# Performance work log

Measured on AMD Instinct MI355X. Metric: run time of the kernel, lower is better.

Reference implementation:

```python
import jax, jax.numpy as jnp
import numpy as np

N_NODES = 2048
N_EDGES = 32768
DIM = 256
HEADS = 4

PARAM_SHAPES = {
    'Wq': (DIM, DIM), 'bq': (DIM,), 'Wk': (DIM, DIM), 'bk': (DIM,),
    'Wv': (DIM, DIM), 'bv': (DIM,), 'Wo': (DIM, DIM), 'bo': (DIM,),
    'gd_W1': (4, 3), 'gd_b1': (3,), 'gd_W2': (3, HEADS), 'gd_b2': (HEADS,),
    'tw_W1': (2 * DIM, DIM), 'tw_b1': (DIM,), 'tw_W2': (DIM, DIM), 'tw_b2': (DIM,),
    'ne_W1': (4 * DIM, 2 * DIM), 'ne_b1': (2 * DIM,), 'ne_W2': (2 * DIM, DIM), 'ne_b2': (DIM,),
    'att_W1': (2 * DIM // HEADS, 2 * DIM // HEADS), 'att_b1': (2 * DIM // HEADS,),
    'att_W2': (DIM // HEADS, 2 * DIM // HEADS), 'att_b2': (DIM // HEADS,),
    'pe_W': (DIM, DIM), 'pe_b': (DIM,), 'pq_W': (DIM, DIM), 'pq_b': (DIM,),
    'pv_W': (DIM, DIM), 'pv_b': (DIM,),
    'pr_W1': (2 * DIM, 2 * DIM), 'pr_b1': (2 * DIM,), 'pr_W2': (2 * DIM, DIM), 'pr_b2': (DIM,),
}


def _lin(x, W, b):
    return x @ W + b


def _mlp2(x, W1, b1, W2, b2):  # Linear-ReLU-Linear (build_mlp, on_last=False)
    return _lin(jnp.maximum(_lin(x, W1, b1), 0.0), W2, b2)


def setup_inputs() -> dict:
    key = jax.random.key(0)
    ks = iter(jax.random.split(key, 64))
    rng = np.random.default_rng(0)
    half = N_EDGES // 2
    s = rng.integers(0, N_NODES, half)
    d = rng.integers(0, N_NODES, half)
    # reciprocal edge pairs so the reverse-edge lookup path is exercised
    edge_index = jnp.asarray(np.stack([np.concatenate([s, d]), np.concatenate([d, s])]), dtype=jnp.int32)
    inp = {
        'node_f': jax.random.normal(next(ks), (N_NODES, DIM), jnp.float32),
        'edge_f': jax.random.normal(next(ks), (N_EDGES, DIM), jnp.float32),
        'coords': jax.random.normal(next(ks), (N_NODES, 3), jnp.float32),
        'edge_index': edge_index,
        'num_heads': HEADS,
    }
    for name, shp in PARAM_SHAPES.items():
        inp[name] = jax.random.normal(next(ks), shp, jnp.float32) * 0.02
    return inp


def _forward(node_f, edge_f, coords, edge_index, num_heads,
             Wq, bq, Wk, bk, Wv, bv, Wo, bo,
             gd_W1, gd_b1, gd_W2, gd_b2,
             tw_W1, tw_b1, tw_W2, tw_b2,
             ne_W1, ne_b1, ne_W2, ne_b2,
             att_W1, att_b1, att_W2, att_b2,
             pe_W, pe_b, pq_W, pq_b, pv_W, pv_b,
             pr_W1, pr_b1, pr_W2, pr_b2):
    N, Dn = node_f.shape
    E, De = edge_f.shape
    H = num_heads
    dh = Wq.shape[1] // H
    src, dst = edge_index[0], edge_index[1]

    # --- NodeUpdate: distance-aware MHSA over all node pairs (batch=1) ---
    q = _lin(node_f, Wq, bq).reshape(N, H, dh)
    k = _lin(node_f, Wk, bk).reshape(N, H, dh)
    v = _lin(node_f, Wv, bv).reshape(N, H, dh)
    diff = coords[:, None, :] - coords[None, :, :]  # [N,N,3]
    sq = jnp.sum(diff * diff, axis=-1, keepdims=True)
    dist = jnp.where(sq > 0, jnp.sqrt(jnp.where(sq > 0, sq, 1.0)), 0.0)
    dmask = _mlp2(jnp.concatenate([diff, dist], -1), gd_W1, gd_b1, gd_W2, gd_b2)  # [N,N,H]
    scores = jnp.einsum('nhd,mhd->hnm', q, k) / float(dh) ** 0.5 + dmask.transpose(2, 0, 1)
    attn = jax.nn.softmax(scores, axis=-1)
    mhsa = _lin(jnp.einsum('hnm,mhd->nhd', attn, v).reshape(N, H * dh), Wo, bo)

    # --- TwinningEdgeAttention: per-node mean of outgoing / incoming edge feats ---
    ones = jnp.ones((E,), edge_f.dtype)
    cnt_s = jnp.maximum(jax.ops.segment_sum(ones, src, num_segments=N), 1.0)
    cnt_d = jnp.maximum(jax.ops.segment_sum(ones, dst, num_segments=N), 1.0)
    sub_mean = jax.ops.segment_sum(edge_f, src, num_segments=N) / cnt_s[:, None]
    obj_mean = jax.ops.segment_sum(edge_f, dst, num_segments=N) / cnt_d[:, None]
    edge_att = jax.nn.sigmoid(_mlp2(jnp.concatenate([sub_mean, obj_mean], -1), tw_W1, tw_b1, tw_W2, tw_b2))
    node_out = jnp.maximum(mhsa, 0.0) * edge_att  # [N, Dn]

    # --- GraphEdgeAttenNetwork ---
    x_i = node_f[src]
    x_j = node_f[dst]
    # reverse-edge matching (vectorized replacement of the python double loop)
    table = jnp.zeros((N * N,), jnp.int32).at[src * N + dst].set(jnp.arange(E, dtype=jnp.int32) + 1)
    rev = table[dst * N + src]
    rev_feat = jnp.where((rev > 0)[:, None], edge_f[jnp.maximum(rev - 1, 0)], 0.0)
    edge_out = _mlp2(jnp.concatenate([x_i, edge_f, rev_feat, x_j], -1), ne_W1, ne_b1, ne_W2, ne_b2)

    value = _lin(x_j, pv_W, pv_b)  # [E, Da]
    query = _lin(x_i, pq_W, pq_b).reshape(E, Dn // H, H)
    edgep = _lin(edge_f, pe_W, pe_b).reshape(E, De // H, H)
    qe = jnp.concatenate([query, edgep], axis=1)  # [E, d_n+d_e, H]
    # conv1d(kernel=1) MLP over channel axis, ReLU between layers
    h = jnp.maximum(jnp.einsum('ech,oc->eoh', qe, att_W1) + att_b1[None, :, None], 0.0)
    prob = jax.nn.softmax(jnp.einsum('ech,oc->eoh', h, att_W2) + att_b2[None, :, None], axis=1)  # [E, d_o, H]
    msg = prob.reshape(E, -1) * value
    agg = jax.ops.segment_max(msg, src, num_segments=N)
    agg = jnp.where(jnp.isfinite(agg), agg, 0.0)  # empty segments -> 0 (torch scatter_max fill)
    xx = _mlp2(jnp.concatenate([node_f, agg], -1), pr_W1, pr_b1, pr_W2, pr_b2)
    return node_out, edge_out, xx


def reference(node_f, edge_f, coords, edge_index, num_heads,
              Wq, bq, Wk, bk, Wv, bv, Wo, bo,
              gd_W1, gd_b1, gd_W2, gd_b2,
              tw_W1, tw_b1, tw_W2, tw_b2,
              ne_W1, ne_b1, ne_W2, ne_b2,
              att_W1, att_b1, att_W2, att_b2,
              pe_W, pe_b, pq_W, pq_b, pv_W, pv_b,
              pr_W1, pr_b1, pr_W2, pr_b2):
    return _forward(node_f, edge_f, coords, edge_index, num_heads,
                    Wq, bq, Wk, bk, Wv, bv, Wo, bo,
                    gd_W1, gd_b1, gd_W2, gd_b2,
                    tw_W1, tw_b1, tw_W2, tw_b2,
                    ne_W1, ne_b1, ne_W2, ne_b2,
                    att_W1, att_b1, att_W2, att_b2,
                    pe_W, pe_b, pq_W, pq_b, pv_W, pv_b,
                    pr_W1, pr_b1, pr_W2, pr_b2)
```

## Files before the change

kernel.cpp:

```cpp
#include <hip/hip_runtime.h>

#define NN 2048
#define NE 32768
#define DIM 256
#define NH 4

typedef unsigned short u16;
typedef __attribute__((ext_vector_type(4))) unsigned short u16x4;
typedef __attribute__((ext_vector_type(8))) short bf16x8;
typedef __attribute__((ext_vector_type(4))) float f32x4;

typedef __attribute__((address_space(1))) const unsigned int g_as1;
typedef __attribute__((address_space(3))) unsigned int l_as3;

__device__ __forceinline__ void gload16(const u16* g, u16* l) {
  __builtin_amdgcn_global_load_lds((g_as1*)g, (l_as3*)l, 16, 0, 0);
}

__device__ __forceinline__ u16 f2bf(float f) {
  unsigned u = __float_as_uint(f);
  unsigned r = u + 0x7FFFu + ((u >> 16) & 1u);
  return (u16)(r >> 16);
}
__device__ __forceinline__ float bf2f(u16 b) {
  return __uint_as_float(((unsigned)b) << 16);
}

struct GB { const u16* A; const int* idx; long ld; long aoffz; };

template<int BNF, int EPI>
__global__ __launch_bounds__(256) void gemm_bf(
    GB ga, const u16* __restrict__ Bt, long bld, long boffz,
    const float* __restrict__ bias, void* __restrict__ Cp, long ldc, long coffz,
    int K, float scale)
{
  __shared__ u16 As[128 * 64];
  __shared__ u16 Bs[32 * BNF * 64];

  const int tid = threadIdx.x;
  const int wid = tid >> 6, lane = tid & 63;
  const int bz = blockIdx.z;
  const int m0 = blockIdx.y * 128;
  const int n0 = blockIdx.x * (32 * BNF);
  const int wr = wid >> 1, wc = wid & 1;
  const int l15 = lane & 15, l4 = lane >> 4;

  const u16* asrc[4];
  #pragma unroll
  for (int c = 0; c < 4; ++c) {
    int rl = c*32 + wid*8 + (lane >> 3);
    int row = ga.idx ? ga.idx[m0 + rl] : (m0 + rl);
    int c16s = (lane & 7) ^ (rl & 7);
    asrc[c] = ga.A + ga.aoffz * bz + (long)row * ga.ld + c16s * 8;
  }
  const u16* bsrc[BNF];
  #pragma unroll
  for (int c = 0; c < BNF; ++c) {
    int rl = c*32 + wid*8 + (lane >> 3);
    int c16s = (lane & 7) ^ (rl & 7);
    bsrc[c] = Bt + boffz * bz + (long)(n0 + rl) * bld + c16s * 8;
  }

  f32x4 acc[4][BNF] = {};

  for (int k0 = 0; k0 < K; k0 += 64) {
    #pragma unroll
    for (int c = 0; c < 4; ++c)
      gload16(asrc[c] + k0, &As[(c*32 + wid*8) * 64]);
    #pragma unroll
    for (int c = 0; c < BNF; ++c)
      gload16(bsrc[c] + k0, &Bs[(c*32 + wid*8) * 64]);
    __syncthreads();

    #pragma unroll
    for (int kk = 0; kk < 2; ++kk) {
      bf16x8 af[4], bfr[BNF];
      #pragma unroll
      for (int i = 0; i < 4; ++i) {
        int r = wr*64 + i*16 + l15;
        af[i] = *(const bf16x8*)&As[r*64 + (((kk*4 + l4) ^ (r & 7)) * 8)];
      }
      #pragma unroll
      for (int j = 0; j < BNF; ++j) {
        int r = wc*(16*BNF) + j*16 + l15;
        bfr[j] = *(const bf16x8*)&Bs[r*64 + (((kk*4 + l4) ^ (r & 7)) * 8)];
      }
      #pragma unroll
      for (int i = 0; i < 4; ++i)
        #pragma unroll
        for (int j = 0; j < BNF; ++j)
          acc[i][j] = __builtin_amdgcn_mfma_f32_16x16x32_bf16(af[i], bfr[j], acc[i][j], 0, 0, 0);
    }
    __syncthreads();
  }

  #pragma unroll
  for (int j = 0; j < BNF; ++j) {
    const int col = n0 + wc*(16*BNF) + j*16 + l15;
    const float bb = bias ? bias[col] : 0.f;
    #pragma unroll
    for (int i = 0; i < 4; ++i) {
      #pragma unroll
      for (int r = 0; r < 4; ++r) {
        const int m = m0 + wr*64 + i*16 + l4*4 + r;
        float v = acc[i][j][r] * scale + bb;
        if constexpr (EPI == 1) v = fmaxf(v, 0.f);
        if constexpr (EPI == 2) v = 1.f / (1.f + expf(-v));
        if constexpr (EPI == 0 || EPI == 2)
          ((float*)Cp)[coffz*bz + (long)m*ldc + col] = v;
        else if constexpr (EPI == 4)
          ((u16*)Cp)[((long)(col & 3) * NE + m) * ldc + (col >> 2) + coffz] = f2bf(v);
        else if constexpr (EPI == 8) {
          if (col < 256)
            ((float*)Cp)[(long)m*256 + (col & 3)*64 + (col >> 2)] = v;
          else {
            u16* qb = (u16*)((float*)Cp + (long)NN*256);
            int c2 = col - 256;
            qb[((long)(c2 & 3)*NN + m)*64 + (c2 >> 2)] = f2bf(v);
          }
        }
        else
          ((u16*)Cp)[coffz*bz + (long)m*ldc + col] = f2bf(v);
      }
    }
  }
}

__global__ __launch_bounds__(256) void flash_k(
    const u16* __restrict__ qkv,
    const u16* __restrict__ vT,
    const float4* __restrict__ pk,
    const float* __restrict__ gW1, const float* __restrict__ gb1,
    const float* __restrict__ gW2, const float* __restrict__ gb2,
    u16* __restrict__ Op,
    float2* __restrict__ ml)
{
  __shared__ u16 Kls[128*64];
  __shared__ u16 Vls[2][64*64];
  __shared__ u16 Pls[4][16*128];

  const int tid = threadIdx.x, wid = tid >> 6, lane = tid & 63;
  const int h  = blockIdx.x & 3;
  const int m0 = (blockIdx.x >> 2) * 64;
  const int part = blockIdx.y;
  const int l15 = lane & 15, l4 = lane >> 4;
  const int rl8 = wid*8 + (lane >> 3);
  const int c8  = lane & 7;

  bf16x8 qf[2];
  {
    const u16* qp = qkv + (long)(m0 + wid*16 + l15)*768 + h*64 + l4*8;
    qf[0] = *(const bf16x8*)(qp);
    qf[1] = *(const bf16x8*)(qp + 32);
  }

  const float b10 = gb1[0], b11 = gb1[1], b12 = gb1[2];
  const float w30 = gW1[9], w31 = gW1[10], w32 = gW1[11];
  const float w20 = gW2[0*4+h], w21 = gW2[1*4+h], w22 = gW2[2*4+h];
  const float b2h = gb2[h];
  float4 rp0[4], rp1[4];
  #pragma unroll
  for (int r = 0; r < 4; ++r) {
    int qrow = m0 + wid*16 + l4*4 + r;
    rp0[r] = pk[qrow*2]; rp1[r] = pk[qrow*2 + 1];
  }

  float mrun[4] = {-1e30f, -1e30f, -1e30f, -1e30f};
  float lrun[4] = {};
  f32x4 pa[4] = {};

  for (int t = 0; t < 2; ++t) {
    const int n0 = part*256 + t*128;
    #pragma unroll
    for (int c = 0; c < 4; ++c) {
      int r = c*32 + rl8;
      gload16(qkv + (long)(n0 + r)*768 + 256 + h*64 + ((c8 ^ (r & 7))*8),
              &Kls[(c*32 + wid*8)*64]);
    }
    #pragma unroll
    for (int hh = 0; hh < 2; ++hh)
      #pragma unroll
      for (int c = 0; c < 2; ++c) {
        int r = c*32 + rl8;
        gload16(vT + (long)(h*64 + r)*NN + n0 + hh*64 + ((c8 ^ (r & 7))*8),
                &Vls[hh][(c*32 + wid*8)*64]);
      }
    __syncthreads();

    f32x4 sa[8] = {};
    #pragma unroll
    for (int kk = 0; kk < 2; ++kk) {
      #pragma unroll
      for (int j = 0; j < 8; ++j) {
        int r = j*16 + l15;
        bf16x8 bf = *(const bf16x8*)&Kls[r*64 + (((kk*4 + l4) ^ (r & 7))*8)];
        sa[j] = __builtin_amdgcn_mfma_f32_16x16x32_bf16(qf[kk], bf, sa[j], 0, 0, 0);
      }
    }

    float rowmx[4] = {-1e30f, -1e30f, -1e30f, -1e30f};
    #pragma unroll
    for (int j = 0; j < 8; ++j) {
      int n = n0 + j*16 + l15;
      float4 cp0 = pk[n*2], cp1 = pk[n*2 + 1];
      #pragma unroll
      for (int r = 0; r < 4; ++r) {
        float dot = rp0[r].x*cp0.x + rp0[r].y*cp0.y + rp0[r].z*cp0.z;
        float sq = rp0[r].w + cp0.w - 2.f*dot;
        float dist = sq > 0.f ? sq * __frsqrt_rn(sq) : 0.f;
        float h0 = fmaxf(b10 + rp1[r].x - cp1.x + dist*w30, 0.f);
        float h1 = fmaxf(b11 + rp1[r].y - cp1.y + dist*w31, 0.f);
        float h2 = fmaxf(b12 + rp1[r].z - cp1.z + dist*w32, 0.f);
        float s = sa[j][r]*0.125f + b2h + h0*w20 + h1*w21 + h2*w22;
        sa[j][r] = s;
        rowmx[r] = fmaxf(rowmx[r], s);
      }
    }
    #pragma unroll
    for (int w = 1; w < 16; w <<= 1)
      #pragma unroll
      for (int r = 0; r < 4; ++r)
        rowmx[r] = fmaxf(rowmx[r], __shfl_xor(rowmx[r], w));

    float fac[4], rs[4] = {};
    #pragma unroll
    for (int r = 0; r < 4; ++r) {
      float mnew = fmaxf(mrun[r], rowmx[r]);
      fac[r] = __expf(mrun[r] - mnew);
      mrun[r] = mnew;
    }
    #pragma unroll
    for (int j = 0; j < 8; ++j)
      #pragma unroll
      for (int r = 0; r < 4; ++r) {
        float p = __expf(sa[j][r] - mrun[r]);
        sa[j][r] = p;
        rs[r] += p;
      }
    #pragma unroll
    for (int w = 1; w < 16; w <<= 1)
      #pragma unroll
      for (int r = 0; r < 4; ++r)
        rs[r] += __shfl_xor(rs[r], w);
    #pragma unroll
    for (int r = 0; r < 4; ++r) lrun[r] = lrun[r]*fac[r] + rs[r];
    #pragma unroll
    for (int j2 = 0; j2 < 4; ++j2)
      #pragma unroll
      for (int r = 0; r < 4; ++r)
        pa[j2][r] *= fac[r];

    #pragma unroll
    for (int j = 0; j < 8; ++j)
      #pragma unroll
      for (int r = 0; r < 4; ++r) {
        int qr = l4*4 + r, n = j*16 + l15;
        Pls[wid][qr*128 + (((n >> 3) ^ (qr & 7))*8) + (n & 7)] = f2bf(sa[j][r]);
      }
    #pragma unroll
    for (int ks = 0; ks < 4; ++ks) {
      bf16x8 paf = *(const bf16x8*)&Pls[wid][l15*128 + (((ks*4 + l4) ^ (l15 & 7))*8)];
      #pragma unroll
      for (int j2 = 0; j2 < 4; ++j2) {
        int r = j2*16 + l15;
        bf16x8 vf = *(const bf16x8*)&Vls[ks >> 1][r*64 + ((((ks & 1)*4 + l4) ^ (r & 7))*8)];
        pa[j2] = __builtin_amdgcn_mfma_f32_16x16x32_bf16(paf, vf, pa[j2], 0, 0, 0);
      }
    }
    __syncthreads();
  }

  #pragma unroll
  for (int j2 = 0; j2 < 4; ++j2)
    #pragma unroll
    for (int r = 0; r < 4; ++r) {
      int m = m0 + wid*16 + l4*4 + r;
      Op[((long)part*NN + m)*256 + h*64 + j2*16 + l15] = f2bf(pa[j2][r]);
    }
  if (l15 == 0) {
    #pragma unroll
    for (int r = 0; r < 4; ++r) {
      int m = m0 + wid*16 + l4*4 + r;
      ml[((long)part*NN + m)*4 + h] = make_float2(mrun[r], lrun[r]);
    }
  }
}

__global__ __launch_bounds__(256) void comb_k(const u16* __restrict__ Op,
    const float2* __restrict__ ml, u16* __restrict__ attn) {
  int n = blockIdx.x, t = threadIdx.x, h = t >> 6;
  float m[8], l[8];
  #pragma unroll
  for (int p = 0; p < 8; ++p) { float2 v = ml[((long)p*NN + n)*4 + h]; m[p] = v.x; l[p] = v.y; }
  float M = m[0];
  #pragma unroll
  for (int p = 1; p < 8; ++p) M = fmaxf(M, m[p]);
  float L = 0.f, o = 0.f;
  #pragma unroll
  for (int p = 0; p < 8; ++p) {
    float w = __expf(m[p] - M);
    L += w * l[p];
    o += w * bf2f(Op[((long)p*NN + n)*256 + t]);
  }
  attn[(long)n*256 + t] = f2bf(o / L);
}

__global__ __launch_bounds__(64) void attedge_k(
    const u16* __restrict__ qN, const u16* __restrict__ ep,
    const float* __restrict__ valNp, const int* __restrict__ ei,
    const u16* __restrict__ W1, const float* __restrict__ b1,
    const u16* __restrict__ W2, const float* __restrict__ b2,
    u16* __restrict__ msgP)
{
  __shared__ u16 As[32*128];
  const int lane = threadIdx.x;
  const int h = blockIdx.y;
  const int e0 = blockIdx.x * 32;
  const int l15 = lane & 15, l4 = lane >> 4;

  #pragma unroll
  for (int p = 0; p < 8; ++p) {
    int R0 = p*4;
    int r  = R0 + (lane >> 4);
    int cd = lane & 15;
    int cs = ((cd & 7) ^ (r & 7)) | (cd & 8);
    const u16* src = (cs < 8)
        ? qN + ((long)h*NN + ei[e0 + r])*64 + cs*8
        : ep + ((long)h*NE + e0 + r)*64 + (cs & 7)*8;
    gload16(src, &As[R0*128]);
  }
  __syncthreads();

  f32x4 acc1[2][8] = {};
  #pragma unroll
  for (int kk = 0; kk < 4; ++kk) {
    bf16x8 af[2], bfr[8];
    #pragma unroll
    for (int i = 0; i < 2; ++i) {
      int rA = i*16 + l15;
      int cg = kk*4 + l4;
      int cd = ((cg & 7) ^ (rA & 7)) | (cg & 8);
      af[i] = *(const bf16x8*)&As[rA*128 + cd*8];
    }
    #pragma unroll
    for (int j = 0; j < 8; ++j)
      bfr[j] = *(const bf16x8*)&W1[(long)(j*16 + l15)*128 + kk*32 + l4*8];
    #pragma unroll
    for (int i = 0; i < 2; ++i)
      #pragma unroll
      for (int j = 0; j < 8; ++j)
        acc1[i][j] = __builtin_amdgcn_mfma_f32_16x16x32_bf16(af[i], bfr[j], acc1[i][j], 0, 0, 0);
  }
  __syncthreads();
  #pragma unroll
  for (int i = 0; i < 2; ++i)
    #pragma unroll
    for (int j = 0; j < 8; ++j) {
      int n = j*16 + l15;
      float bb = b1[n];
      #pragma unroll
      for (int r = 0; r < 4; ++r) {
        int m = i*16 + l4*4 + r;
        int cg = n >> 3;
        int cd = ((cg & 7) ^ (m & 7)) | (cg & 8);
        As[m*128 + cd*8 + (n & 7)] = f2bf(fmaxf(acc1[i][j][r] + bb, 0.f));
      }
    }
  __syncthreads();

  f32x4 acc2[2][4] = {};
  #pragma unroll
  for (int kk = 0; kk < 4; ++kk) {
    bf16x8 af[2], bfr[4];
    #pragma unroll
    for (int i = 0; i < 2; ++i) {
      int rA = i*16 + l15;
      int cg = kk*4 + l4;
      int cd = ((cg & 7) ^ (rA & 7)) | (cg & 8);
      af[i] = *(const bf16x8*)&As[rA*128 + cd*8];
    }
    #pragma unroll
    for (int j = 0; j < 4; ++j)
      bfr[j] = *(const bf16x8*)&W2[(long)(j*16 + l15)*128 + kk*32 + l4*8];
    #pragma unroll
    for (int i = 0; i < 2; ++i)
      #pragma unroll
      for (int j = 0; j < 4; ++j)
        acc2[i][j] = __builtin_amdgcn_mfma_f32_16x16x32_bf16(af[i], bfr[j], acc2[i][j], 0, 0, 0);
  }

  #pragma unroll
  for (int i = 0; i < 2; ++i) {
    float mx[4] = {-1e30f,-1e30f,-1e30f,-1e30f};
    #pragma unroll
    for (int j = 0; j < 4; ++j) {
      float bb = b2[j*16 + l15];
      #pragma unroll
      for (int r = 0; r < 4; ++r) {
        acc2[i][j][r] += bb;
        mx[r] = fmaxf(mx[r], acc2[i][j][r]);
      }
    }
    #pragma unroll
    for (int w = 1; w < 16; w <<= 1)
      #pragma unroll
      for (int r = 0; r < 4; ++r) mx[r] = fmaxf(mx[r], __shfl_xor(mx[r], w));
    float sum[4] = {};
    #pragma unroll
    for (int j = 0; j < 4; ++j)
      #pragma unroll
      for (int r = 0; r < 4; ++r) {
        float p = __expf(acc2[i][j][r] - mx[r]);
        acc2[i][j][r] = p; sum[r] += p;
      }
    #pragma unroll
    for (int w = 1; w < 16; w <<= 1)
      #pragma unroll
      for (int r = 0; r < 4; ++r) sum[r] += __shfl_xor(sum[r], w);
    #pragma unroll
    for (int r = 0; r < 4; ++r) {
      int m = i*16 + l4*4 + r;
      int e = e0 + m;
      int dst = ei[NE + e];
      float inv = 1.f / sum[r];
      #pragma unroll
      for (int j = 0; j < 4; ++j) {
        int o = j*16 + l15;
        float v = valNp[(long)dst*256 + h*64 + o];
        msgP[(long)e*256 + h*64 + o] = f2bf(acc2[i][j][r] * inv * v);
      }
    }
  }
}

__global__ __launch_bounds__(512) void gemm_ne(
    const u16* __restrict__ nbf, const u16* __restrict__ ebf, const u16* __restrict__ zbuf,
    const int* __restrict__ ei, const int* __restrict__ rev,
    const u16* __restrict__ Bt, const float* __restrict__ bias, u16* __restrict__ C)
{
  __shared__ u16 As[2][128 * 64];
  __shared__ u16 Bs[2][128 * 64];
  const int tid = threadIdx.x, wid = tid >> 6, lane = tid & 63;
  const int lin = blockIdx.y * 4 + blockIdx.x;
  const int xcd = lin & 7, seq = lin >> 3;
  const int m0 = (xcd*32 + (seq >> 2)) * 128;
  const int n0 = (seq & 3) * 128;
  const int wr = wid >> 2, wc = wid & 3, l15 = lane & 15, l4 = lane >> 4;

  const u16* asrc[4][2];
  #pragma unroll
  for (int c = 0; c < 2; ++c) {
    int rl = c*64 + wid*8 + (lane >> 3);
    int m = m0 + rl;
    int c16s = ((lane & 7) ^ (rl & 7)) * 8;
    int si = ei[m], di = ei[NE + m], rv = rev[m];
    asrc[0][c] = nbf + (long)si * 256 + c16s;
    asrc[1][c] = ebf + (long)m * 256 + c16s;
    asrc[2][c] = (rv >= 0 ? ebf + (long)rv * 256 : zbuf) + c16s;
    asrc[3][c] = nbf + (long)di * 256 + c16s;
  }
  const u16* bsrc[2];
  #pragma unroll
  for (int c = 0; c < 2; ++c) {
    int rl = c*64 + wid*8 + (lane >> 3);
    int c16s = (lane & 7) ^ (rl & 7);
    bsrc[c] = Bt + (long)(n0 + rl) * 1024 + c16s * 8;
  }

  f32x4 acc[4][2] = {};

#define NE_STAGE(BUF, IT) do {                                                  \
    const int seg_ = (IT) >> 2, kt_ = (IT) & 3;                                 \
    _Pragma("unroll")                                                           \
    for (int c = 0; c < 2; ++c)                                                 \
      gload16(asrc[seg_][c] + kt_*64, &As[BUF][(c*64 + wid*8) * 64]);           \
    _Pragma("unroll")                                                           \
    for (int c = 0; c < 2; ++c)                                                 \
      gload16(bsrc[c] + seg_*256 + kt_*64, &Bs[BUF][(c*64 + wid*8) * 64]);      \
  } while (0)

  NE_STAGE(0, 0);
  #pragma unroll
  for (int it = 0; it < 16; ++it) {
    const int b = it & 1;
    if (it < 15) {
      NE_STAGE(b ^ 1, it + 1);
      asm volatile("s_waitcnt vmcnt(4)" ::: "memory");
    } else {
      asm volatile("s_waitcnt vmcnt(0)" ::: "memory");
    }
    __builtin_amdgcn_s_barrier();
    asm volatile("" ::: "memory");
    #pragma unroll
    for (int kk = 0; kk < 2; ++kk) {
      bf16x8 af[4], bfr[2];
      #pragma unroll
      for (int i = 0; i < 4; ++i) {
        int r = wr*64 + i*16 + l15;
        af[i] = *(const bf16x8*)&As[b][r*64 + (((kk*4 + l4) ^ (r & 7)) * 8)];
      }
      #pragma unroll
      for (int j = 0; j < 2; ++j) {
        int r = wc*32 + j*16 + l15;
        bfr[j] = *(const bf16x8*)&Bs[b][r*64 + (((kk*4 + l4) ^ (r & 7)) * 8)];
      }
      #pragma unroll
      for (int i = 0; i < 4; ++i)
        #pragma unroll
        for (int j = 0; j < 2; ++j)
          acc[i][j] = __builtin_amdgcn_mfma_f32_16x16x32_bf16(af[i], bfr[j], acc[i][j], 0, 0, 0);
    }
    asm volatile("" ::: "memory");
    __builtin_amdgcn_s_barrier();
  }
#undef NE_STAGE

  #pragma unroll
  for (int j = 0; j < 2; ++j) {
    const int col = n0 + wc*32 + j*16 + l15;
    const float bb = bias[col];
    #pragma unroll
    for (int i = 0; i < 4; ++i) {
      #pragma unroll
      for (int r = 0; r < 4; ++r) {
        const int m = m0 + wr*64 + i*16 + l4*4 + r;
        C[(long)m*512 + col] = f2bf(fmaxf(acc[i][j][r] + bb, 0.f));
      }
    }
  }
}

struct PrepEnt { const float* src; void* dst; int K; int N; int ntiles; int op; };
struct PrepDesc { PrepEnt e[24]; int n; };

__global__ __launch_bounds__(256) void wprep_k(PrepDesc d) {
  __shared__ float t[32][33];
  int b = blockIdx.x;
  int ei = 0;
  while (ei < d.n && b >= d.e[ei].ntiles) { b -= d.e[ei].ntiles; ++ei; }
  if (ei >= d.n) return;
  PrepEnt E = d.e[ei];
  int tid = threadIdx.x;
  if (E.op == 0) {
    int kt = E.K >> 5;
    int bk = (b % kt) * 32, bn = (b / kt) * 32;
    int tx = tid & 31, ty = tid >> 5;
    #pragma unroll
    for (int i = ty; i < 32; i += 8) t[i][tx] = E.src[(long)(bk + i) * E.N + bn + tx];
    __syncthreads();
    u16* dst = (u16*)E.dst;
    #pragma unroll
    for (int i = ty; i < 32; i += 8) dst[(long)(bn + i) * E.K + bk + tx] = f2bf(t[tx][i]);
  } else if (E.op == 1) {
    long i = (long)b * 256 + tid;
    long n4 = ((long)E.K * E.N) >> 2;
    if (i < n4) {
      float4 v = ((const float4*)E.src)[i];
      u16x4 o = { f2bf(v.x), f2bf(v.y), f2bf(v.z), f2bf(v.w) };
      ((u16x4*)E.dst)[i] = o;
    }
  } else if (E.op == 3) {
    long i = (long)b * 256 + tid;
    long n4 = ((long)E.K * E.N) >> 2;
    if (i < n4) {
      float4 v = ((const float4*)E.src)[i];
      long row = i >> 6;
      long col = (i & 63) * 4;
      u16x4 o = { f2bf(v.x), f2bf(v.y), f2bf(v.z), f2bf(v.w) };
      *(u16x4*)((u16*)E.dst + row*512 + col) = o;
    }
  } else {
    int i = b * 256 + tid;
    if (i < E.N) ((float*)E.dst)[i] = E.src[i];
  }
}

__global__ void geo_k(const float* __restrict__ C3, const float* __restrict__ gW1,
                      float* __restrict__ geo) {
  int n = blockIdx.x * 256 + threadIdx.x;
  if (n >= NN) return;
  float cx = C3[3*n], cy = C3[3*n+1], cz = C3[3*n+2];
  float s = cx*cx + cy*cy + cz*cz;
  float a0 = cx*gW1[0] + cy*gW1[3] + cz*gW1[6];
  float a1 = cx*gW1[1] + cy*gW1[4] + cz*gW1[7];
  float a2 = cx*gW1[2] + cy*gW1[5] + cz*gW1[8];
  float4* g = (float4*)(geo + (long)n*8);
  g[0] = make_float4(cx, cy, cz, s);
  g[1] = make_float4(a0, a1, a2, 0.f);
}

__global__ __launch_bounds__(256) void transb_k(const u16* __restrict__ src,
                                                u16* __restrict__ dst) {
  __shared__ u16 t[32][34];
  int bm = blockIdx.x * 32, bc = blockIdx.y * 32;
  int tx = threadIdx.x & 31, ty = threadIdx.x >> 5;
  #pragma unroll
  for (int i = ty; i < 32; i += 8) t[i][tx] = src[(long)(bm+i)*768 + 512 + bc + tx];
  __syncthreads();
  #pragma unroll
  for (int i = ty; i < 32; i += 8) dst[(long)(bc+i)*NN + bm + tx] = t[tx][i];
}

__global__ void count_k(const int* __restrict__ ei, int* __restrict__ cs,
                        int* __restrict__ cd) {
  int e = blockIdx.x * 256 + threadIdx.x;
  atomicAdd(&cs[ei[e]], 1);
  atomicAdd(&cd[ei[NE + e]], 1);
}

__global__ __launch_bounds__(256) void scan2_k(const int* __restrict__ cnt_all,
    int* __restrict__ start_all, int* __restrict__ cursor_all) {
  const int* cnt = cnt_all + blockIdx.x * NN;
  int* start  = start_all + blockIdx.x * (NN + 1);
  int* cursor = cursor_all + blockIdx.x * NN;
  __shared__ int part[256];
  int t = threadIdx.x;
  int loc[8]; int s = 0;
  #pragma unroll
  for (int i = 0; i < 8; ++i) { int v = cnt[t*8 + i]; loc[i] = s; s += v; }
  part[t] = s;
  __syncthreads();
  if (t == 0) { int a = 0; for (int i = 0; i < 256; ++i) { int v = part[i]; part[i] = a; a += v; } }
  __syncthreads();
  int base = part[t];
  #pragma unroll
  for (int i = 0; i < 8; ++i) { start[t*8+i] = base + loc[i]; cursor[t*8+i] = base + loc[i]; }
  if (t == 255) start[NN] = base + s;
}

__global__ void scatter2_k(const int* __restrict__ ei, int* __restrict__ cur_s,
    int* __restrict__ cur_d, int* __restrict__ eids_s, int* __restrict__ eids_d) {
  int e = blockIdx.x * 256 + threadIdx.x;
  int p = atomicAdd(&cur_s[ei[e]], 1);
  eids_s[p] = e;
  int q = atomicAdd(&cur_d[ei[NE + e]], 1);
  eids_d[q] = e;
}

__global__ void rev2_k(const int* __restrict__ ei, const int* __restrict__ start_s,
    const int* __restrict__ eids_s, int* __restrict__ rev) {
  int e = blockIdx.x * 256 + threadIdx.x;
  int s = ei[e], d = ei[NE + e];
  int b = start_s[d], en = start_s[d+1];
  int best = -1;
  for (int i = b; i < en; ++i) {
    int e2 = eids_s[i];
    if (ei[NE + e2] == s) best = max(best, e2);
  }
  rev[e] = best;
}

__global__ __launch_bounds__(256) void twmean_k(const u16* __restrict__ ebf,
    const int* __restrict__ start_s, const int* __restrict__ eids_s,
    const int* __restrict__ start_d, const int* __restrict__ eids_d,
    u16* __restrict__ twA)
{
  int n = blockIdx.x, t = threadIdx.x, role = blockIdx.y;
  const int* start = role ? start_d : start_s;
  const int* eids  = role ? eids_d  : eids_s;
  int b0 = start[n], e0 = start[n+1];
  float s = 0.f;
  for (int i = b0; i < e0; ++i)
    s += bf2f(ebf[(long)eids[i]*256 + t]);
  twA[(long)n*512 + role*256 + t] = f2bf(s / fmaxf((float)(e0 - b0), 1.f));
}

__global__ void node_out_k(const float* mh, const float* ea, float* out) {
  long i = (long)blockIdx.x * 256 + threadIdx.x;
  out[i] = fmaxf(mh[i], 0.f) * ea[i];
}

__global__ __launch_bounds__(256) void agg_k(const int* __restrict__ start,
    const int* __restrict__ eids, const u16* __restrict__ msgP, u16* __restrict__ prA) {
  int n = blockIdx.x, t = threadIdx.x;
  int b = start[n], e_ = start[n+1];
  float mx = -1e30f;
  for (int i = b; i < e_; ++i) {
    int e = eids[i];
    mx = fmaxf(mx, bf2f(msgP[(long)e*256 + t]));
  }
  int c = (t & 63) * 4 + (t >> 6);
  prA[(long)n*512 + 256 + c] = (e_ > b) ? f2bf(mx) : f2bf(0.f);
}

static GB gb(const u16* A, const int* idx, long ld, long aoffz) {
  GB g; g.A = A; g.idx = idx; g.ld = ld; g.aoffz = aoffz; return g;
}

extern "C" void kernel_launch(void* const* d_in, const int* in_sizes, int n_in,
                              void* d_out, int out_size, void* d_ws, size_t ws_size,
                              hipStream_t stream) {
  (void)in_sizes; (void)n_in; (void)out_size; (void)ws_size;

  const float* node_f = (const float*)d_in[0];
  const float* edge_f = (const float*)d_in[1];
  const float* coords = (const float*)d_in[2];
  const int*   ei     = (const int*)d_in[3];
  const float* Wq = (const float*)d_in[5];  const float* bq = (const float*)d_in[6];
  const float* Wk = (const float*)d_in[7];  const float* bk = (const float*)d_in[8];
  const float* Wv = (const float*)d_in[9];  const float* bv = (const float*)d_in[10];
  const float* Wo = (const float*)d_in[11]; const float* bo = (const float*)d_in[12];
  const float* gd_W1 = (const float*)d_in[13]; const float* gd_b1 = (const float*)d_in[14];
  const float* gd_W2 = (const float*)d_in[15]; const float* gd_b2 = (const float*)d_in[16];
  const float* tw_W1 = (const float*)d_in[17]; const float* tw_b1 = (const float*)d_in[18];
  const float* tw_W2 = (const float*)d_in[19]; const float* tw_b2 = (const float*)d_in[20];
  const float* ne_W1 = (const float*)d_in[21]; const float* ne_b1 = (const float*)d_in[22];
  const float* ne_W2 = (const float*)d_in[23]; const float* ne_b2 = (const float*)d_in[24];
  const float* att_W1 = (const float*)d_in[25]; const float* att_b1 = (const float*)d_in[26];
  const float* att_W2 = (const float*)d_in[27]; const float* att_b2 = (const float*)d_in[28];
  const float* pe_W = (const float*)d_in[29]; const float* pe_b = (const float*)d_in[30];
  const float* pq_W = (const float*)d_in[31]; const float* pq_b = (const float*)d_in[32];
  const float* pv_W = (const float*)d_in[33]; const float* pv_b = (const float*)d_in[34];
  const float* pr_W1 = (const float*)d_in[35]; const float* pr_b1 = (const float*)d_in[36];
  const float* pr_W2 = (const float*)d_in[37]; const float* pr_b2 = (const float*)d_in[38];

  char* WB = (char*)d_ws;
  float* out = (float*)d_out;
  float* out_node = out;
  float* out_edge = out + (long)NN*DIM;
  float* out_xx   = out + (long)NN*DIM + (long)NE*DIM;

  const long sz_R1 = 4L*NN*NN*4;
  const long sz_R2 = 4L*NN*NN*2;
  const long sz_R3 = 4L*NE*128*2;
  const long R1 = 0, R2 = R1 + sz_R1, R3 = R2 + sz_R2;

  u16*    Opart = (u16*)(WB + R1);
  float2* mlbuf = (float2*)(WB + R1 + 8L*NN*256*2);
  u16*    msgP  = (u16*)(WB + R1);
  u16*   nehid  = (u16*)(WB + R2);
  u16*   ep     = (u16*)(WB + R3);
  u16*   edge_bf= (u16*)(WB + R3 + (long)NN*NN*4);

  long cur = R3 + sz_R3;
  auto alloc = [&](long bytes) { long o = cur; cur += (bytes + 255) & ~255L; return o; };

  long o_sub = alloc((long)NN*768*2 + (long)NN*DIM*2 + (long)NN*DIM*2);
  u16* qkv_bf  = (u16*)(WB + o_sub);
  u16* vT      = qkv_bf + (long)NN*768;
  u16* attn_bf = vT + (long)NN*DIM;

  long o_cs  = alloc(2L*NN*4);
  int* cs_i = (int*)(WB + o_cs); int* cd_i = cs_i + NN;
  long o_mh  = alloc((long)NN*DIM*4);  float* mhsa = (float*)(WB + o_mh);
  long o_ea  = alloc((long)NN*DIM*4);  float* eatt = (float*)(WB + o_ea);
  long o_rv  = alloc((long)NE*4);      int* rev = (int*)(WB + o_rv);
  long o_st  = alloc(2L*(NN+1)*4);     int* start_s = (int*)(WB + o_st);
  int* start_d = start_s + (NN + 1);
  long o_cu  = alloc(2L*NN*4);         int* cursor_s = (int*)(WB + o_cu);
  int* cursor_d = cursor_s + NN;
  long o_eid = alloc(2L*NE*4);         int* eids_s = (int*)(WB + o_eid);
  int* eids_d = eids_s + NE;
  long o_zb  = alloc(1024);            u16* zbuf = (u16*)(WB + o_zb);
  long o_geo = alloc((long)NN*8*4);    float* geo = (float*)(WB + o_geo);
  long o_nbf = alloc((long)NN*DIM*2);  u16* node_bf = (u16*)(WB + o_nbf);
  long o_twA = alloc((long)NN*512*2);  u16* twA = (u16*)(WB + o_twA);
  long o_twh = alloc((long)NN*DIM*2);  u16* twh = (u16*)(WB + o_twh);
  long o_prA = alloc((long)NN*512*2);  u16* prA = (u16*)(WB + o_prA);
  long o_prh = alloc((long)NN*512*2);  u16* prh = (u16*)(WB + o_prh);
  long o_vN  = alloc((long)NN*256*4 + 4L*NN*64*2);
  float* valN = (float*)(WB + o_vN);
  u16*   qN   = (u16*)(valN + (long)NN*256);

  u16* qkv_t = (u16*)(WB + alloc(3L*DIM*DIM*2));
  u16* Wo_t  = (u16*)(WB + alloc(DIM*DIM*2));
  u16* tw1_t = (u16*)(WB + alloc(DIM*512*2));
  u16* tw2_t = (u16*)(WB + alloc(DIM*DIM*2));
  u16* ne1_t = (u16*)(WB + alloc(512L*1024*2));
  u16* ne2_t = (u16*)(WB + alloc(DIM*512*2));
  u16* pe_t  = (u16*)(WB + alloc(DIM*DIM*2));
  u16* pvq_t = (u16*)(WB + alloc(2L*DIM*DIM*2));
  u16* pr1_t = (u16*)(WB + alloc(512L*512*2));
  u16* pr2_t = (u16*)(WB + alloc(DIM*512*2));
  u16* a1_bf = (u16*)(WB + alloc(128*128*2));
  u16* a2_bf = (u16*)(WB + alloc(64*128*2));
  float* qkvb = (float*)(WB + alloc(768*4));
  float* pvqb = (float*)(WB + alloc(512*4));

  hipMemsetAsync(cs_i, 0, 2L*NN*4, stream);
  hipMemsetAsync(zbuf, 0, 1024, stream);

  PrepDesc pd{}; int ne_ = 0; int tot = 0;
  auto addT = [&](const float* s, u16* d, int K, int N) {
    pd.e[ne_] = { s, d, K, N, (K/32)*(N/32), 0 }; tot += pd.e[ne_].ntiles; ++ne_;
  };
  auto addC = [&](const float* s, u16* d, long elems) {
    int nt = (int)((elems/4 + 255) / 256);
    pd.e[ne_] = { s, d, 1, (int)elems, nt, 1 }; tot += nt; ++ne_;
  };
  auto addB = [&](const float* s, float* d, int n) {
    pd.e[ne_] = { s, d, 1, n, (n + 255)/256, 2 }; tot += pd.e[ne_].ntiles; ++ne_;
  };
  addT(Wq, qkv_t,               DIM, DIM);
  addT(Wk, qkv_t + DIM*DIM,     DIM, DIM);
  addT(Wv, qkv_t + 2*DIM*DIM,   DIM, DIM);
  addT(Wo, Wo_t, DIM, DIM);
  addT(tw_W1, tw1_t, 512, DIM);
  addT(tw_W2, tw2_t, DIM, DIM);
  addT(ne_W1, ne1_t, 1024, 512);
  addT(ne_W2, ne2_t, 512, DIM);
  addT(pe_W, pe_t, DIM, DIM);
  addT(pv_W, pvq_t,             DIM, DIM);
  addT(pq_W, pvq_t + DIM*DIM,   DIM, DIM);
  addT(pr_W1, pr1_t, 512, 512);
  addT(pr_W2, pr2_t, 512, DIM);
  addC(att_W1, a1_bf, 128*128);
  addC(att_W2, a2_bf, 64*128);
  addC(node_f, node_bf, (long)NN*DIM);
  addC(edge_f, edge_bf, (long)NE*DIM);
  addB(bq, qkvb, 256); addB(bk, qkvb + 256, 256); addB(bv, qkvb + 512, 256);
  addB(pv_b, pvqb, 256); addB(pq_b, pvqb + 256, 256);
  pd.e[ne_] = { node_f, prA, NN, 256, (int)(((long)NN*256/4 + 255)/256), 3 };
  tot += pd.e[ne_].ntiles; ++ne_;
  pd.n = ne_;
  wprep_k<<<tot, 256, 0, stream>>>(pd);
  geo_k<<<NN/256, 256, 0, stream>>>(coords, gd_W1, geo);

  count_k<<<NE/256, 256, 0, stream>>>(ei, cs_i, cd_i);
  scan2_k<<<2, 256, 0, stream>>>(cs_i, start_s, cursor_s);
  scatter2_k<<<NE/256, 256, 0, stream>>>(ei, cursor_s, cursor_d, eids_s, eids_d);
  rev2_k<<<NE/256, 256, 0, stream>>>(ei, start_s, eids_s, rev);
  twmean_k<<<dim3(NN,2), 256, 0, stream>>>(edge_bf, start_s, eids_s, start_d, eids_d, twA);
  gemm_bf<4,1><<<dim3(2,16,1), 256, 0, stream>>>(gb(twA, nullptr, 512, 0), tw1_t, 512, 0,
      tw_b1, twh, DIM, 0, 512, 1.f);
  gemm_bf<4,2><<<dim3(2,16,1), 256, 0, stream>>>(gb(twh, nullptr, DIM, 0), tw2_t, DIM, 0,
      tw_b2, eatt, DIM, 0, DIM, 1.f);

  gemm_bf<4,5><<<dim3(6,16,1), 256, 0, stream>>>(gb(node_bf, nullptr, DIM, 0), qkv_t, DIM, 0,
      qkvb, qkv_bf, 768, 0, DIM, 1.f);
  transb_k<<<dim3(64,8), 256, 0, stream>>>(qkv_bf, vT);
  flash_k<<<dim3(128,8), 256, 0, stream>>>(qkv_bf, vT, (const float4*)geo,
      gd_W1, gd_b1, gd_W2, gd_b2, Opart, mlbuf);
  comb_k<<<NN, 256, 0, stream>>>(Opart, mlbuf, attn_bf);
  gemm_bf<4,0><<<dim3(2,16,1), 256, 0, stream>>>(gb(attn_bf, nullptr, DIM, 0), Wo_t, DIM, 0,
      bo, mhsa, DIM, 0, DIM, 1.f);
  node_out_k<<<NN, 256, 0, stream>>>(mhsa, eatt, out_node);

  gemm_ne<<<dim3(4,256,1), 512, 0, stream>>>(node_bf, edge_bf, zbuf, ei, rev,
      ne1_t, ne_b1, nehid);
  gemm_bf<4,0><<<dim3(2,256,1), 256, 0, stream>>>(gb(nehid, nullptr, 512, 0), ne2_t, 512, 0,
      ne_b2, out_edge, DIM, 0, 512, 1.f);

  gemm_bf<4,8><<<dim3(4,16,1), 256, 0, stream>>>(gb(node_bf, nullptr, DIM, 0), pvq_t, DIM, 0,
      pvqb, valN, 256, 0, DIM, 1.f);
  gemm_bf<4,4><<<dim3(2,256,1), 256, 0, stream>>>(gb(edge_bf, nullptr, DIM, 0), pe_t, DIM, 0,
      pe_b, ep, 64, 0, DIM, 1.f);
  attedge_k<<<dim3(NE/32, NH), 64, 0, stream>>>(qN, ep, valN, ei,
      a1_bf, att_b1, a2_bf, att_b2, msgP);
  agg_k<<<NN, 256, 0, stream>>>(start_s, eids_s, msgP, prA);

  gemm_bf<4,1><<<dim3(4,16,1), 256, 0, stream>>>(gb(prA, nullptr, 512, 0), pr1_t, 512, 0,
      pr_b1, prh, 512, 0, 512, 1.f);
  gemm_bf<4,0><<<dim3(2,16,1), 256, 0, stream>>>(gb(prh, nullptr, 512, 0), pr2_t, 512, 0,
      pr_b2, out_xx, DIM, 0, 512, 1.f);
}
```

Before: 380.6 us.

## Split flash attention into 16 key partitions, fuse node output epilogue

```diff
diff --git a/kernel.cpp b/kernel.cpp
--- a/kernel.cpp
+++ b/kernel.cpp
@@ -32,7 +32,7 @@
 __global__ __launch_bounds__(256) void gemm_bf(
     GB ga, const u16* __restrict__ Bt, long bld, long boffz,
     const float* __restrict__ bias, void* __restrict__ Cp, long ldc, long coffz,
-    int K, float scale)
+    int K, float scale, const float* __restrict__ extra)
 {
   __shared__ u16 As[128 * 64];
   __shared__ u16 Bs[32 * BNF * 64];
@@ -106,7 +106,11 @@
         float v = acc[i][j][r] * scale + bb;
         if constexpr (EPI == 1) v = fmaxf(v, 0.f);
         if constexpr (EPI == 2) v = 1.f / (1.f + expf(-v));
-        if constexpr (EPI == 0 || EPI == 2)
+        if constexpr (EPI == 9) {
+          v = fmaxf(v, 0.f) * extra[(long)m*ldc + col];
+          ((float*)Cp)[(long)m*ldc + col] = v;
+        }
+        else if constexpr (EPI == 0 || EPI == 2)
           ((float*)Cp)[coffz*bz + (long)m*ldc + col] = v;
         else if constexpr (EPI == 4)
           ((u16*)Cp)[((long)(col & 3) * NE + m) * ldc + (col >> 2) + coffz] = f2bf(v);
@@ -165,109 +169,92 @@
     rp0[r] = pk[qrow*2]; rp1[r] = pk[qrow*2 + 1];
   }
 
-  float mrun[4] = {-1e30f, -1e30f, -1e30f, -1e30f};
-  float lrun[4] = {};
   f32x4 pa[4] = {};
-
-  for (int t = 0; t < 2; ++t) {
-    const int n0 = part*256 + t*128;
-    #pragma unroll
-    for (int c = 0; c < 4; ++c) {
+  const int n0 = part*128;
+
+  #pragma unroll
+  for (int c = 0; c < 4; ++c) {
+    int r = c*32 + rl8;
+    gload16(qkv + (long)(n0 + r)*768 + 256 + h*64 + ((c8 ^ (r & 7))*8),
+            &Kls[(c*32 + wid*8)*64]);
+  }
+  #pragma unroll
+  for (int hh = 0; hh < 2; ++hh)
+    #pragma unroll
+    for (int c = 0; c < 2; ++c) {
       int r = c*32 + rl8;
-      gload16(qkv + (long)(n0 + r)*768 + 256 + h*64 + ((c8 ^ (r & 7))*8),
-              &Kls[(c*32 + wid*8)*64]);
-    }
-    #pragma unroll
-    for (int hh = 0; hh < 2; ++hh)
-      #pragma unroll
-      for (int c = 0; c < 2; ++c) {
-        int r = c*32 + rl8;
-        gload16(vT + (long)(h*64 + r)*NN + n0 + hh*64 + ((c8 ^ (r & 7))*8),
-                &Vls[hh][(c*32 + wid*8)*64]);
-      }
-    __syncthreads();
-
-    f32x4 sa[8] = {};
-    #pragma unroll
-    for (int kk = 0; kk < 2; ++kk) {
-      #pragma unroll
-      for (int j = 0; j < 8; ++j) {
-        int r = j*16 + l15;
-        bf16x8 bf = *(const bf16x8*)&Kls[r*64 + (((kk*4 + l4) ^ (r & 7))*8)];
-        sa[j] = __builtin_amdgcn_mfma_f32_16x16x32_bf16(qf[kk], bf, sa[j], 0, 0, 0);
-      }
-    }
-
-    float rowmx[4] = {-1e30f, -1e30f, -1e30f, -1e30f};
+      gload16(vT + (long)(h*64 + r)*NN + n0 + hh*64 + ((c8 ^ (r & 7))*8),
+              &Vls[hh][(c*32 + wid*8)*64]);
+    }
+  __syncthreads();
+
+  f32x4 sa[8] = {};
+  #pragma unroll
+  for (int kk = 0; kk < 2; ++kk) {
     #pragma unroll
     for (int j = 0; j < 8; ++j) {
-      int n = n0 + j*16 + l15;
-      float4 cp0 = pk[n*2], cp1 = pk[n*2 + 1];
-      #pragma unroll
-      for (int r = 0; r < 4; ++r) {
-        float dot = rp0[r].x*cp0.x + rp0[r].y*cp0.y + rp0[r].z*cp0.z;
-        float sq = rp0[r].w + cp0.w - 2.f*dot;
-        float dist = sq > 0.f ? sq * __frsqrt_rn(sq) : 0.f;
-        float h0 = fmaxf(b10 + rp1[r].x - cp1.x + dist*w30, 0.f);
-        float h1 = fmaxf(b11 + rp1[r].y - cp1.y + dist*w31, 0.f);
-        float h2 = fmaxf(b12 + rp1[r].z - cp1.z + dist*w32, 0.f);
-        float s = sa[j][r]*0.125f + b2h + h0*w20 + h1*w21 + h2*w22;
-        sa[j][r] = s;
-        rowmx[r] = fmaxf(rowmx[r], s);
-      }
-    }
-    #pragma unroll
-    for (int w = 1; w < 16; w <<= 1)
-      #pragma unroll
-      for (int r = 0; r < 4; ++r)
-        rowmx[r] = fmaxf(rowmx[r], __shfl_xor(rowmx[r], w));
-
-    float fac[4], rs[4] = {};
+      int r = j*16 + l15;
+      bf16x8 bf = *(const bf16x8*)&Kls[r*64 + (((kk*4 + l4) ^ (r & 7))*8)];
+      sa[j] = __builtin_amdgcn_mfma_f32_16x16x32_bf16(qf[kk], bf, sa[j], 0, 0, 0);
+    }
+  }
+
+  float rowmx[4] = {-1e30f, -1e30f, -1e30f, -1e30f};
+  #pragma unroll
+  for (int j = 0; j < 8; ++j) {
+    int n = n0 + j*16 + l15;
+    float4 cp0 = pk[n*2], cp1 = pk[n*2 + 1];
     #pragma unroll
     for (int r = 0; r < 4; ++r) {
-      float mnew = fmaxf(mrun[r], rowmx[r]);
-      fac[r] = __expf(mrun[r] - mnew);
-      mrun[r] = mnew;
-    }
-    #pragma unroll
-    for (int j = 0; j < 8; ++j)
-      #pragma unroll
-      for (int r = 0; r < 4; ++r) {
-        float p = __expf(sa[j][r] - mrun[r]);
-        sa[j][r] = p;
-        rs[r] += p;
-      }
-    #pragma unroll
-    for (int w = 1; w < 16; w <<= 1)
-      #pragma unroll
-      for (int r = 0; r < 4; ++r)
-        rs[r] += __shfl_xor(rs[r], w);
-    #pragma unroll
-    for (int r = 0; r < 4; ++r) lrun[r] = lrun[r]*fac[r] + rs[r];
-    #pragma unroll
-    for (int j2 = 0; j2 < 4; ++j2)
-      #pragma unroll
-      for (int r = 0; r < 4; ++r)
-        pa[j2][r] *= fac[r];
-
-    #pragma unroll
-    for (int j = 0; j < 8; ++j)
-      #pragma unroll
-      for (int r = 0; r < 4; ++r) {
-        int qr = l4*4 + r, n = j*16 + l15;
-        Pls[wid][qr*128 + (((n >> 3) ^ (qr & 7))*8) + (n & 7)] = f2bf(sa[j][r]);
-      }
-    #pragma unroll
-    for (int ks = 0; ks < 4; ++ks) {
-      bf16x8 paf = *(const bf16x8*)&Pls[wid][l15*128 + (((ks*4 + l4) ^ (l15 & 7))*8)];
-      #pragma unroll
-      for (int j2 = 0; j2 < 4; ++j2) {
-        int r = j2*16 + l15;
-        bf16x8 vf = *(const bf16x8*)&Vls[ks >> 1][r*64 + ((((ks & 1)*4 + l4) ^ (r & 7))*8)];
-        pa[j2] = __builtin_amdgcn_mfma_f32_16x16x32_bf16(paf, vf, pa[j2], 0, 0, 0);
-      }
-    }
-    __syncthreads();
+      float dot = rp0[r].x*cp0.x + rp0[r].y*cp0.y + rp0[r].z*cp0.z;
+      float sq = rp0[r].w + cp0.w - 2.f*dot;
+      float dist = sq > 0.f ? sq * __frsqrt_rn(sq) : 0.f;
+      float h0 = fmaxf(b10 + rp1[r].x - cp1.x + dist*w30, 0.f);
+      float h1 = fmaxf(b11 + rp1[r].y - cp1.y + dist*w31, 0.f);
+      float h2 = fmaxf(b12 + rp1[r].z - cp1.z + dist*w32, 0.f);
+      float s = sa[j][r]*0.125f + b2h + h0*w20 + h1*w21 + h2*w22;
+      sa[j][r] = s;
+      rowmx[r] = fmaxf(rowmx[r], s);
+    }
+  }
+  #pragma unroll
+  for (int w = 1; w < 16; w <<= 1)
+    #pragma unroll
+    for (int r = 0; r < 4; ++r)
+      rowmx[r] = fmaxf(rowmx[r], __shfl_xor(rowmx[r], w));
+
+  float rs[4] = {};
+  #pragma unroll
+  for (int j = 0; j < 8; ++j)
+    #pragma unroll
+    for (int r = 0; r < 4; ++r) {
+      float p = __expf(sa[j][r] - rowmx[r]);
+      sa[j][r] = p;
+      rs[r] += p;
+    }
+  #pragma unroll
+  for (int w = 1; w < 16; w <<= 1)
+    #pragma unroll
+    for (int r = 0; r < 4; ++r)
+      rs[r] += __shfl_xor(rs[r], w);
+
+  #pragma unroll
+  for (int j = 0; j < 8; ++j)
+    #pragma unroll
+    for (int r = 0; r < 4; ++r) {
+      int qr = l4*4 + r, n = j*16 + l15;
+      Pls[wid][qr*128 + (((n >> 3) ^ (qr & 7))*8) + (n & 7)] = f2bf(sa[j][r]);
+    }
+  asm volatile("" ::: "memory");
+  #pragma unroll
+  for (int ks = 0; ks < 4; ++ks) {
+    bf16x8 paf = *(const bf16x8*)&Pls[wid][l15*128 + (((ks*4 + l4) ^ (l15 & 7))*8)];
+    #pragma unroll
+    for (int j2 = 0; j2 < 4; ++j2) {
+      int r = j2*16 + l15;
+      bf16x8 vf = *(const bf16x8*)&Vls[ks >> 1][r*64 + ((((ks & 1)*4 + l4) ^ (r & 7))*8)];
+      pa[j2] = __builtin_amdgcn_mfma_f32_16x16x32_bf16(paf, vf, pa[j2], 0, 0, 0);
+    }
   }
 
   #pragma unroll
@@ -281,7 +268,7 @@
     #pragma unroll
     for (int r = 0; r < 4; ++r) {
       int m = m0 + wid*16 + l4*4 + r;
-      ml[((long)part*NN + m)*4 + h] = make_float2(mrun[r], lrun[r]);
+      ml[((long)part*NN + m)*4 + h] = make_float2(rowmx[r], rs[r]);
     }
   }
 }
@@ -289,15 +276,15 @@
 __global__ __launch_bounds__(256) void comb_k(const u16* __restrict__ Op,
     const float2* __restrict__ ml, u16* __restrict__ attn) {
   int n = blockIdx.x, t = threadIdx.x, h = t >> 6;
-  float m[8], l[8];
-  #pragma unroll
-  for (int p = 0; p < 8; ++p) { float2 v = ml[((long)p*NN + n)*4 + h]; m[p] = v.x; l[p] = v.y; }
+  float m[16], l[16];
+  #pragma unroll
+  for (int p = 0; p < 16; ++p) { float2 v = ml[((long)p*NN + n)*4 + h]; m[p] = v.x; l[p] = v.y; }
   float M = m[0];
   #pragma unroll
-  for (int p = 1; p < 8; ++p) M = fmaxf(M, m[p]);
+  for (int p = 1; p < 16; ++p) M = fmaxf(M, m[p]);
   float L = 0.f, o = 0.f;
   #pragma unroll
-  for (int p = 0; p < 8; ++p) {
+  for (int p = 0; p < 16; ++p) {
     float w = __expf(m[p] - M);
     L += w * l[p];
     o += w * bf2f(Op[((long)p*NN + n)*256 + t]);
@@ -305,7 +292,7 @@
   attn[(long)n*256 + t] = f2bf(o / L);
 }
 
-__global__ __launch_bounds__(64) void attedge_k(
+__global__ __launch_bounds__(64, 5) void attedge_k(
     const u16* __restrict__ qN, const u16* __restrict__ ep,
     const float* __restrict__ valNp, const int* __restrict__ ei,
     const u16* __restrict__ W1, const float* __restrict__ b1,
@@ -663,11 +650,6 @@
   for (int i = b0; i < e0; ++i)
     s += bf2f(ebf[(long)eids[i]*256 + t]);
   twA[(long)n*512 + role*256 + t] = f2bf(s / fmaxf((float)(e0 - b0), 1.f));
-}
-
-__global__ void node_out_k(const float* mh, const float* ea, float* out) {
-  long i = (long)blockIdx.x * 256 + threadIdx.x;
-  out[i] = fmaxf(mh[i], 0.f) * ea[i];
 }
 
 __global__ __launch_bounds__(256) void agg_k(const int* __restrict__ start,
@@ -726,7 +708,7 @@
   const long R1 = 0, R2 = R1 + sz_R1, R3 = R2 + sz_R2;
 
   u16*    Opart = (u16*)(WB + R1);
-  float2* mlbuf = (float2*)(WB + R1 + 8L*NN*256*2);
+  float2* mlbuf = (float2*)(WB + R1 + 16L*NN*256*2);
   u16*    msgP  = (u16*)(WB + R1);
   u16*   nehid  = (u16*)(WB + R2);
   u16*   ep     = (u16*)(WB + R3);
@@ -742,7 +724,6 @@
 
   long o_cs  = alloc(2L*NN*4);
   int* cs_i = (int*)(WB + o_cs); int* cd_i = cs_i + NN;
-  long o_mh  = alloc((long)NN*DIM*4);  float* mhsa = (float*)(WB + o_mh);
   long o_ea  = alloc((long)NN*DIM*4);  float* eatt = (float*)(WB + o_ea);
   long o_rv  = alloc((long)NE*4);      int* rev = (int*)(WB + o_rv);
   long o_st  = alloc(2L*(NN+1)*4);     int* start_s = (int*)(WB + o_st);
@@ -822,35 +803,34 @@
   rev2_k<<<NE/256, 256, 0, stream>>>(ei, start_s, eids_s, rev);
   twmean_k<<<dim3(NN,2), 256, 0, stream>>>(edge_bf, start_s, eids_s, start_d, eids_d, twA);
   gemm_bf<4,1><<<dim3(2,16,1), 256, 0, stream>>>(gb(twA, nullptr, 512, 0), tw1_t, 512, 0,
-      tw_b1, twh, DIM, 0, 512, 1.f);
+      tw_b1, twh, DIM, 0, 512, 1.f, nullptr);
   gemm_bf<4,2><<<dim3(2,16,1), 256, 0, stream>>>(gb(twh, nullptr, DIM, 0), tw2_t, DIM, 0,
-      tw_b2, eatt, DIM, 0, DIM, 1.f);
+      tw_b2, eatt, DIM, 0, DIM, 1.f, nullptr);
 
   gemm_bf<4,5><<<dim3(6,16,1), 256, 0, stream>>>(gb(node_bf, nullptr, DIM, 0), qkv_t, DIM, 0,
-      qkvb, qkv_bf, 768, 0, DIM, 1.f);
+      qkvb, qkv_bf, 768, 0, DIM, 1.f, nullptr);
   transb_k<<<dim3(64,8), 256, 0, stream>>>(qkv_bf, vT);
-  flash_k<<<dim3(128,8), 256, 0, stream>>>(qkv_bf, vT, (const float4*)geo,
+  flash_k<<<dim3(128,16), 256, 0, stream>>>(qkv_bf, vT, (const float4*)geo,
       gd_W1, gd_b1, gd_W2, gd_b2, Opart, mlbuf);
   comb_k<<<NN, 256, 0, stream>>>(Opart, mlbuf, attn_bf);
-  gemm_bf<4,0><<<dim3(2,16,1), 256, 0, stream>>>(gb(attn_bf, nullptr, DIM, 0), Wo_t, DIM, 0,
-      bo, mhsa, DIM, 0, DIM, 1.f);
-  node_out_k<<<NN, 256, 0, stream>>>(mhsa, eatt, out_node);
+  gemm_bf<4,9><<<dim3(2,16,1), 256, 0, stream>>>(gb(attn_bf, nullptr, DIM, 0), Wo_t, DIM, 0,
+      bo, out_node, DIM, 0, DIM, 1.f, eatt);
 
   gemm_ne<<<dim3(4,256,1), 512, 0, stream>>>(node_bf, edge_bf, zbuf, ei, rev,
       ne1_t, ne_b1, nehid);
   gemm_bf<4,0><<<dim3(2,256,1), 256, 0, stream>>>(gb(nehid, nullptr, 512, 0), ne2_t, 512, 0,
-      ne_b2, out_edge, DIM, 0, 512, 1.f);
+      ne_b2, out_edge, DIM, 0, 512, 1.f, nullptr);
 
   gemm_bf<4,8><<<dim3(4,16,1), 256, 0, stream>>>(gb(node_bf, nullptr, DIM, 0), pvq_t, DIM, 0,
-      pvqb, valN, 256, 0, DIM, 1.f);
+      pvqb, valN, 256, 0, DIM, 1.f, nullptr);
   gemm_bf<4,4><<<dim3(2,256,1), 256, 0, stream>>>(gb(edge_bf, nullptr, DIM, 0), pe_t, DIM, 0,
-      pe_b, ep, 64, 0, DIM, 1.f);
+      pe_b, ep, 64, 0, DIM, 1.f, nullptr);
   attedge_k<<<dim3(NE/32, NH), 64, 0, stream>>>(qN, ep, valN, ei,
       a1_bf, att_b1, a2_bf, att_b2, msgP);
   agg_k<<<NN, 256, 0, stream>>>(start_s, eids_s, msgP, prA);
 
   gemm_bf<4,1><<<dim3(4,16,1), 256, 0, stream>>>(gb(prA, nullptr, 512, 0), pr1_t, 512, 0,
-      pr_b1, prh, 512, 0, 512, 1.f);
+      pr_b1, prh, 512, 0, 512, 1.f, nullptr);
   gemm_bf<4,0><<<dim3(2,16,1), 256, 0, stream>>>(gb(prh, nullptr, 512, 0), pr2_t, 512, 0,
-      pr_b2, out_xx, DIM, 0, 512, 1.f);
-}
+      pr_b2, out_xx, DIM, 0, 512, 1.f, nullptr);
+}
```

Result: slower. 400.6 us (+5.3%).
